# Kernel optimization log

Hardware: AMD Instinct MI355X
Metric: run time of the kernel (lower is better)

## Reference

```python
import jax, jax.numpy as jnp
import numpy as np

TOPK = 1024
C = 32
FC0 = 256
EPS_BN = 1e-5
EPS_NORM = 1e-12


def setup_inputs() -> dict:
    key = jax.random.key(0)
    ks = jax.random.split(key, 8)
    B, L = 128, 16384
    N = B * L
    x = jax.random.normal(ks[0], (N, C), dtype=jnp.float32)
    length = jnp.full((B,), L, dtype=jnp.int32)
    # conv1d_1: Conv1d(32, 1, 1) -> weight [1, 32, 1] ~ vector [32], bias [1]
    w_att = jax.random.normal(ks[1], (C,), dtype=jnp.float32) * (1.0 / np.sqrt(C))
    b_att = jnp.zeros((1,), dtype=jnp.float32)
    # bn_1: BatchNorm1d(1) (eval mode: use running stats)
    g1 = jnp.ones((1,), dtype=jnp.float32)
    be1 = jnp.zeros((1,), dtype=jnp.float32)
    rm1 = jnp.zeros((1,), dtype=jnp.float32)
    rv1 = jnp.ones((1,), dtype=jnp.float32)
    # fc_1: Linear(TOPK*C, FC0)
    fan_in = TOPK * C
    W_fc = jax.random.normal(ks[2], (FC0, fan_in), dtype=jnp.float32) * (1.0 / np.sqrt(fan_in))
    b_fc = jnp.zeros((FC0,), dtype=jnp.float32)
    # bn_2: BatchNorm1d(FC0) (eval mode)
    g2 = jnp.ones((FC0,), dtype=jnp.float32)
    be2 = jnp.zeros((FC0,), dtype=jnp.float32)
    rm2 = jnp.zeros((FC0,), dtype=jnp.float32)
    rv2 = jnp.ones((FC0,), dtype=jnp.float32)
    return {"x": x, "length": length, "w_att": w_att, "b_att": b_att,
            "g1": g1, "be1": be1, "rm1": rm1, "rv1": rv1,
            "W_fc": W_fc, "b_fc": b_fc,
            "g2": g2, "be2": be2, "rm2": rm2, "rv2": rv2}


def reference(x, length, w_att, b_att, g1, be1, rm1, rv1, W_fc, b_fc, g2, be2, rm2, rv2):
    B = length.shape[0]
    N = x.shape[0]
    L = N // B  # equal-length segments (sum(length) == N)
    # attention score: 1x1 conv over channels + BatchNorm1d(1) (eval)
    att = x @ w_att + b_att[0]                                   # [N]
    att = (att - rm1[0]) * (g1[0] / jnp.sqrt(rv1[0] + EPS_BN)) + be1[0]
    # per-segment descending sort + take top TOPK == top_k per segment
    att_b = att.reshape(B, L)                                    # [B, L]
    x_b = x.reshape(B, L, C)                                     # [B, L, C]
    _, idx = jax.lax.top_k(att_b, TOPK)                          # [B, TOPK]
    ranked = jnp.take_along_axis(x_b, idx[:, :, None], axis=1)   # [B, TOPK, C]
    flat = ranked.reshape(B, TOPK * C)                           # [B, TOPK*C]
    # fc_1 + bn_2 (eval) + L2 row-normalize
    out = flat @ W_fc.T + b_fc                                   # [B, FC0]
    out = (out - rm2) * (g2 / jnp.sqrt(rv2 + EPS_BN)) + be2
    nrm = jnp.maximum(jnp.linalg.norm(out, axis=1, keepdims=True), EPS_NORM)
    return out / nrm
```

## Files before the change

kernel.cpp:

```cpp
#include <hip/hip_runtime.h>
#include <stdint.h>

#define CC 32
#define TOPK 1024
#define FC0 256

__global__ __launch_bounds__(256)
void k_att(const float* __restrict__ x,
           const float* __restrict__ w_att, const float* __restrict__ b_att,
           uint32_t* __restrict__ key, int N)
{
    __shared__ float tile[256][CC + 1];
    const int t = threadIdx.x;
    const size_t base = (size_t)blockIdx.x * 256;
    const float4* xv = (const float4*)(x + base * CC);
    #pragma unroll
    for (int i = 0; i < 8; ++i) {
        int e = i * 256 + t;
        float4 v = xv[e];
        int r = e >> 3, c4 = (e & 7) * 4;
        tile[r][c4 + 0] = v.x; tile[r][c4 + 1] = v.y;
        tile[r][c4 + 2] = v.z; tile[r][c4 + 3] = v.w;
    }
    __syncthreads();
    float p[8];
    #pragma unroll
    for (int j = 0; j < 8; ++j) {
        float pj = __fmul_rn(tile[t][j], w_att[j]);
        pj = __fmaf_rn(tile[t][8 + j],  w_att[8 + j],  pj);
        pj = __fmaf_rn(tile[t][16 + j], w_att[16 + j], pj);
        pj = __fmaf_rn(tile[t][24 + j], w_att[24 + j], pj);
        p[j] = pj;
    }
    float q0 = __fadd_rn(p[0], p[1]);
    float q1 = __fadd_rn(p[2], p[3]);
    float q2 = __fadd_rn(p[4], p[5]);
    float q3 = __fadd_rn(p[6], p[7]);
    float dot = __fadd_rn(__fadd_rn(q0, q1), __fadd_rn(q2, q3));
    float v = __fadd_rn(dot, b_att[0]);
    uint32_t bits = __float_as_uint(v);
    key[base + t] = (bits & 0x80000000u) ? ~bits : (bits | 0x80000000u);
}

__global__ __launch_bounds__(1024)
void k_topk(const uint32_t* __restrict__ key, int* __restrict__ idx_out, int L)
{
    __shared__ uint32_t kv[16384];
    __shared__ uint64_t cv[2048];
    __shared__ uint32_t hist[257];
    __shared__ uint32_t s_prefix, s_k, s_cnt;
    const int t = threadIdx.x;
    const int b = blockIdx.x;
    const int lane = t & 63;
    const uint32_t* kseg = key + (size_t)b * L;
    for (int i = t; i < L; i += 1024) kv[i] = kseg[i];
    if (t == 0) { s_prefix = 0; s_k = TOPK; s_cnt = 0; }
    __syncthreads();
    for (int r = 3; r >= 0; --r) {
        if (t < 257) hist[t] = 0;
        __syncthreads();
        const uint32_t pref = s_prefix;
        const uint32_t k = s_k;
        const int sh = r * 8;
        for (int i = t; i < L; i += 1024) {
            uint32_t u = kv[i];
            if (r == 3 || (u >> (sh + 8)) == pref)
                atomicAdd(&hist[(u >> sh) & 255u], 1u);
        }
        __syncthreads();
        #pragma unroll
        for (int off = 1; off < 256; off <<= 1) {
            uint32_t v = 0;
            if (t < 256 && t + off < 256) v = hist[t + off];
            __syncthreads();
            if (t < 256) hist[t] += v;
            __syncthreads();
        }
        if (t < 256) {
            uint32_t st = hist[t], sn = hist[t + 1];
            if (st >= k && sn < k) {
                s_prefix = (pref << 8) | (uint32_t)t;
                s_k = k - sn;
            }
        }
        __syncthreads();
    }
    const uint32_t T = s_prefix;
    for (int i = t; i < L; i += 1024) {
        bool q = kv[i] >= T;
        unsigned long long m = __ballot(q);
        uint32_t base = 0;
        if (lane == 0 && m)
            base = atomicAdd(&s_cnt, (uint32_t)__popcll(m));
        base = __shfl(base, 0);
        if (q) {
            uint32_t pos = base + (uint32_t)__popcll(m & ((1ULL << lane) - 1ULL));
            if (pos < 2048)
                cv[pos] = ((uint64_t)kv[i] << 32) | (uint64_t)(uint32_t)(~(uint32_t)i);
        }
    }
    __syncthreads();
    const uint32_t mm = s_cnt < 2048u ? s_cnt : 2048u;
    for (int i = t; i < 2048; i += 1024)
        if ((uint32_t)i >= mm) cv[i] = 0ULL;
    for (int size = 2; size <= 2048; size <<= 1) {
        for (int stride = size >> 1; stride > 0; stride >>= 1) {
            __syncthreads();
            int i = ((t & ~(stride - 1)) << 1) | (t & (stride - 1));
            int j = i | stride;
            uint64_t va = cv[i], vb = cv[j];
            bool up = ((i & size) == 0);
            if (up ? (va > vb) : (va < vb)) { cv[i] = vb; cv[j] = va; }
        }
    }
    __syncthreads();
    if (t < TOPK)
        idx_out[(size_t)b * TOPK + t] = (int)(~(uint32_t)cv[2047 - t]);
}

#define FT 128
#define KCI 32
#define NKC 128
#define KCHUNK 256

__global__ __launch_bounds__(256)
void k_fc(const float* __restrict__ x, const int* __restrict__ idx,
          const float* __restrict__ W, float* __restrict__ part, int L)
{
    __shared__ float flT[KCI][128];
    __shared__ float wT[KCI][FT];
    const int t = threadIdx.x;
    const int kc = blockIdx.x;
    const int fb = blockIdx.y * FT;
    const int tb = t >> 4, tf = t & 15;
    float acc[8][8];
    #pragma unroll
    for (int i = 0; i < 8; ++i)
        #pragma unroll
        for (int j = 0; j < 8; ++j) acc[i][j] = 0.f;

    const int b_ld = t >> 1, half = t & 1;
    for (int sub = 0; sub < KCHUNK / KCI; ++sub) {
        const int kbase = kc * KCHUNK + sub * KCI;
        const int t_idx = kbase >> 5;
        {
            int row = idx[b_ld * TOPK + t_idx];
            row = row < 0 ? 0 : (row >= L ? L - 1 : row);
            const float* src = x + ((size_t)b_ld * L + row) * CC + half * 16;
            #pragma unroll
            for (int q = 0; q < 4; ++q) {
                float4 v = ((const float4*)src)[q];
                int c0 = half * 16 + q * 4;
                flT[c0 + 0][b_ld] = v.x; flT[c0 + 1][b_ld] = v.y;
                flT[c0 + 2][b_ld] = v.z; flT[c0 + 3][b_ld] = v.w;
            }
        }
        #pragma unroll
        for (int i2 = 0; i2 < 4; ++i2) {
            int fl = (t >> 3) + i2 * 32;
            int u = t & 7;
            const float4 v = *(const float4*)(W + (size_t)(fb + fl) * (TOPK * CC) + kbase + u * 4);
            wT[u * 4 + 0][fl] = v.x; wT[u * 4 + 1][fl] = v.y;
            wT[u * 4 + 2][fl] = v.z; wT[u * 4 + 3][fl] = v.w;
        }
        __syncthreads();
        #pragma unroll
        for (int kk = 0; kk < KCI; ++kk) {
            float bb[8], ww[8];
            *(float4*)&bb[0] = *(const float4*)&flT[kk][tb * 8];
            *(float4*)&bb[4] = *(const float4*)&flT[kk][tb * 8 + 4];
            *(float4*)&ww[0] = *(const float4*)&wT[kk][tf * 8];
            *(float4*)&ww[4] = *(const float4*)&wT[kk][tf * 8 + 4];
            #pragma unroll
            for (int i = 0; i < 8; ++i)
                #pragma unroll
                for (int j = 0; j < 8; ++j)
                    acc[i][j] = fmaf(bb[i], ww[j], acc[i][j]);
        }
        __syncthreads();
    }
    float* pbase = part + ((size_t)kc * 128) * 256 + fb + tf * 8;
    #pragma unroll
    for (int i = 0; i < 8; ++i) {
        float* dst = pbase + (size_t)(tb * 8 + i) * 256;
        ((float4*)dst)[0] = make_float4(acc[i][0], acc[i][1], acc[i][2], acc[i][3]);
        ((float4*)dst)[1] = make_float4(acc[i][4], acc[i][5], acc[i][6], acc[i][7]);
    }
}

__global__ __launch_bounds__(256)
void k_post(const float* __restrict__ part, const float* __restrict__ b_fc,
            const float* __restrict__ g2, const float* __restrict__ be2,
            const float* __restrict__ rm2, const float* __restrict__ rv2,
            float* __restrict__ out)
{
    __shared__ float red[256];
    const int b = blockIdx.x, f = threadIdx.x;
    float s = 0.f;
    #pragma unroll 8
    for (int kc = 0; kc < NKC; ++kc)
        s += part[((size_t)kc * 128 + b) * 256 + f];
    s += b_fc[f];
    float o = (s - rm2[f]) * (g2[f] / sqrtf(rv2[f] + 1e-5f)) + be2[f];
    red[f] = o * o;
    __syncthreads();
    for (int st = 128; st > 0; st >>= 1) {
        if (f < st) red[f] += red[f + st];
        __syncthreads();
    }
    float nrm = fmaxf(sqrtf(red[0]), 1e-12f);
    out[(size_t)b * 256 + f] = o / nrm;
}

extern "C" void kernel_launch(void* const* d_in, const int* in_sizes, int n_in,
                              void* d_out, int out_size, void* d_ws, size_t ws_size,
                              hipStream_t stream)
{
    const float* x     = (const float*)d_in[0];
    const float* w_att = (const float*)d_in[2];
    const float* b_att = (const float*)d_in[3];
    const float* W_fc  = (const float*)d_in[8];
    const float* b_fc  = (const float*)d_in[9];
    const float* g2    = (const float*)d_in[10];
    const float* be2   = (const float*)d_in[11];
    const float* rm2   = (const float*)d_in[12];
    const float* rv2   = (const float*)d_in[13];

    const int N = in_sizes[0] / CC;
    const int B = in_sizes[1];
    const int L = N / B;

    uint8_t* ws = (uint8_t*)d_ws;
    uint32_t* key = (uint32_t*)(ws);
    int* idx      = (int*)(ws + (size_t)N * 4);
    float* part   = (float*)(ws + (size_t)N * 4 + (size_t)B * TOPK * 4);

    k_att<<<N / 256, 256, 0, stream>>>(x, w_att, b_att, key, N);
    k_topk<<<B, 1024, 0, stream>>>(key, idx, L);
    dim3 g3(NKC, FC0 / FT);
    k_fc<<<g3, 256, 0, stream>>>(x, idx, W_fc, part, L);
    k_post<<<B, 256, 0, stream>>>(part, b_fc, g2, be2, rm2, rv2, (float*)d_out);
}
```

Measured before the change: 129.6 us.

## Use per-wavefront radix histograms and shuffle-based bitonic stages in top-k

The radix-select histogram is now built in 16 per-wavefront sub-histograms and summed afterwards, which cuts LDS atomic contention. The bitonic sort of the 2048 candidates runs every stage with stride below 64 in registers using wavefront xor-shuffles, so it needs far fewer block-wide barriers and shared-memory round trips. In exchange it clears a larger shared histogram each radix pass and adds a reduction step.

```diff
diff --git a/kernel.cpp b/kernel.cpp
--- a/kernel.cpp
+++ b/kernel.cpp
@@ -42,22 +42,33 @@
     key[base + t] = (bits & 0x80000000u) ? ~bits : (bits | 0x80000000u);
 }
 
+__device__ __forceinline__ uint64_t cex(uint64_t v, int s, bool up, int t)
+{
+    uint64_t o = (uint64_t)__shfl_xor((unsigned long long)v, s, 64);
+    bool left = ((t & s) == 0);
+    uint64_t mn = v < o ? v : o;
+    uint64_t mx = v < o ? o : v;
+    return (left == up) ? mn : mx;
+}
+
 __global__ __launch_bounds__(1024)
 void k_topk(const uint32_t* __restrict__ key, int* __restrict__ idx_out, int L)
 {
     __shared__ uint32_t kv[16384];
     __shared__ uint64_t cv[2048];
+    __shared__ uint32_t whist[16][257];
     __shared__ uint32_t hist[257];
     __shared__ uint32_t s_prefix, s_k, s_cnt;
     const int t = threadIdx.x;
     const int b = blockIdx.x;
     const int lane = t & 63;
+    const int wid = t >> 6;
     const uint32_t* kseg = key + (size_t)b * L;
     for (int i = t; i < L; i += 1024) kv[i] = kseg[i];
     if (t == 0) { s_prefix = 0; s_k = TOPK; s_cnt = 0; }
     __syncthreads();
     for (int r = 3; r >= 0; --r) {
-        if (t < 257) hist[t] = 0;
+        for (int i = t; i < 16 * 257; i += 1024) (&whist[0][0])[i] = 0;
         __syncthreads();
         const uint32_t pref = s_prefix;
         const uint32_t k = s_k;
@@ -65,8 +76,15 @@
         for (int i = t; i < L; i += 1024) {
             uint32_t u = kv[i];
             if (r == 3 || (u >> (sh + 8)) == pref)
-                atomicAdd(&hist[(u >> sh) & 255u], 1u);
-        }
+                atomicAdd(&whist[wid][(u >> sh) & 255u], 1u);
+        }
+        __syncthreads();
+        if (t < 256) {
+            uint32_t s = 0;
+            #pragma unroll
+            for (int w = 0; w < 16; ++w) s += whist[w][t];
+            hist[t] = s;
+        } else if (t == 256) hist[256] = 0;
         __syncthreads();
         #pragma unroll
         for (int off = 1; off < 256; off <<= 1) {
@@ -103,17 +121,46 @@
     const uint32_t mm = s_cnt < 2048u ? s_cnt : 2048u;
     for (int i = t; i < 2048; i += 1024)
         if ((uint32_t)i >= mm) cv[i] = 0ULL;
-    for (int size = 2; size <= 2048; size <<= 1) {
-        for (int stride = size >> 1; stride > 0; stride >>= 1) {
+    __syncthreads();
+    {
+        uint64_t r0 = cv[t], r1 = cv[t + 1024];
+        #pragma unroll
+        for (int size = 2; size <= 64; size <<= 1) {
+            bool up = ((t & size) == 0);
+            #pragma unroll
+            for (int s = size >> 1; s > 0; s >>= 1) {
+                r0 = cex(r0, s, up, t);
+                r1 = cex(r1, s, up, t);
+            }
+        }
+        cv[t] = r0; cv[t + 1024] = r1;
+    }
+    #pragma unroll
+    for (int size = 128; size <= 2048; size <<= 1) {
+        for (int s = size >> 1; s >= 64; s >>= 1) {
             __syncthreads();
-            int i = ((t & ~(stride - 1)) << 1) | (t & (stride - 1));
-            int j = i | stride;
+            int i = ((t & ~(s - 1)) << 1) | (t & (s - 1));
+            int j = i | s;
             uint64_t va = cv[i], vb = cv[j];
             bool up = ((i & size) == 0);
             if (up ? (va > vb) : (va < vb)) { cv[i] = vb; cv[j] = va; }
         }
-    }
-    __syncthreads();
+        __syncthreads();
+        {
+            uint64_t a0 = cv[t], a1 = cv[t + 1024];
+            bool up0, up1;
+            if (size <= 512)      { up0 = ((t & size) == 0); up1 = up0; }
+            else if (size == 1024){ up0 = true;  up1 = false; }
+            else                  { up0 = true;  up1 = true;  }
+            #pragma unroll
+            for (int s = 32; s > 0; s >>= 1) {
+                a0 = cex(a0, s, up0, t);
+                a1 = cex(a1, s, up1, t);
+            }
+            cv[t] = a0; cv[t + 1024] = a1;
+        }
+        __syncthreads();
+    }
     if (t < TOPK)
         idx_out[(size_t)b * TOPK + t] = (int)(~(uint32_t)cv[2047 - t]);
 }
```

New measurement: 129.8 us. No clear change (+0.1%).
